# Kernel tuning notes

Measured on AMD Instinct MI355X. Metric: run time of the kernel, lower is better.

## Reference

```python
import math
import jax, jax.numpy as jnp
import numpy as np

ORIG_FREQ = 16000
NEW_FREQ = 14400
LPF_WIDTH = 6


def _kaldi_weights(orig_freq, new_freq, lpf_width):
    """Kaldi LinearResample SetIndexesAndWeights (numpy, static)."""
    base = math.gcd(orig_freq, new_freq)
    output_samples = new_freq // base
    min_freq = min(orig_freq, new_freq)
    lowpass_cutoff = 0.99 * 0.5 * min_freq
    window_width = lpf_width / (2.0 * lowpass_cutoff)
    output_t = np.arange(output_samples, dtype=np.float64) / new_freq
    min_t = output_t - window_width
    max_t = output_t + window_width
    min_input_index = np.ceil(min_t * orig_freq)
    max_input_index = np.floor(max_t * orig_freq)
    num_indices = max_input_index - min_input_index + 1
    max_weight_width = int(num_indices.max())
    j = np.arange(max_weight_width, dtype=np.float64)
    input_index = min_input_index[:, None] + j[None, :]
    delta_t = input_index / orig_freq - output_t[:, None]
    weights = np.zeros_like(delta_t)
    inside = np.abs(delta_t) < window_width
    weights[inside] = 0.5 * (1 + np.cos(2 * math.pi * lowpass_cutoff / lpf_width * delta_t[inside]))
    t_zero = delta_t == 0.0
    t_nz = ~t_zero
    weights[t_nz] *= np.sin(2 * math.pi * lowpass_cutoff * delta_t[t_nz]) / (math.pi * delta_t[t_nz])
    weights[t_zero] *= 2 * lowpass_cutoff
    weights /= orig_freq
    return min_input_index.astype(np.int64), weights.astype(np.float32)


def _output_samples(input_num_samp, orig_freq, new_freq):
    tick_freq = abs(orig_freq * new_freq) // math.gcd(orig_freq, new_freq)
    ticks_per_input = tick_freq // orig_freq
    interval_length = input_num_samp * ticks_per_input
    if interval_length <= 0:
        return 0
    ticks_per_output = tick_freq // new_freq
    last = interval_length // ticks_per_output
    if last * ticks_per_output == interval_length:
        last -= 1
    return last + 1


def setup_inputs() -> dict:
    key = jax.random.key(0)
    waveforms = jax.random.normal(key, (64, 480000), dtype=jnp.float32)
    return {"waveforms": waveforms}


def reference(waveforms) -> jnp.ndarray:
    B, T = waveforms.shape
    base = math.gcd(ORIG_FREQ, NEW_FREQ)
    conv_stride = ORIG_FREQ // base          # input samples per unit (10)
    up = NEW_FREQ // base                    # output phases (9)
    first_indices, weights_np = _kaldi_weights(ORIG_FREQ, NEW_FREQ, LPF_WIDTH)
    window_size = weights_np.shape[1]
    tot_out = _output_samples(T, ORIG_FREQ, NEW_FREQ)
    max_index = (tot_out - 1) // up
    end_index = max_index * conv_stride + window_size

    x3 = waveforms[:, None, :]  # [B, 1, T]
    out = jnp.zeros((B, tot_out), dtype=waveforms.dtype)
    dn = jax.lax.conv_dimension_numbers((B, 1, T), (1, 1, window_size), ('NCH', 'OIH', 'NCH'))
    for i in range(up):
        fi = int(first_indices[i])
        start = max(0, fi)
        left_pad = max(0, -fi)
        cur_len = T - fi
        right_pad = max(0, end_index + 1 - cur_len)
        xw = jnp.pad(x3[..., start:], ((0, 0), (0, 0), (left_pad, right_pad)))
        ker = jnp.asarray(weights_np[i], dtype=waveforms.dtype)[None, None, :]
        cw = jax.lax.conv_general_dilated(xw, ker, (conv_stride,), 'VALID', dimension_numbers=dn)[:, 0, :]
        # place phase-i outputs at positions i, i+up, i+2*up, ... < tot_out
        count = (tot_out - i + up - 1) // up
        cw = cw[:, :count]
        if cw.shape[1] < count:
            cw = jnp.pad(cw, ((0, 0), (0, count - cw.shape[1])))
        out = out.at[:, i::up].add(cw)
    return out
```

## Files before the change

### kernel.cpp

```cpp
#include <hip/hip_runtime.h>
#include <math.h>

#define T_IN        480000
#define OUT_PER_ROW 432000
#define K_TOT       48000
#define GPB         256
#define LDS_FLOATS  2576
#define OUT_LDS     (GPB * 9)

struct ResampleW { float w[9][14]; };

__global__ __launch_bounds__(256)
void SpeedPerturb_resample_kernel(const float* __restrict__ in,
                                  float* __restrict__ out,
                                  ResampleW args)
{
    __shared__ float lin[LDS_FLOATS];
    __shared__ float lout[OUT_LDS];
    const int row = blockIdx.y;
    const int k0  = blockIdx.x * GPB;
    const int t   = threadIdx.x;
    const int is0 = 10 * k0 - 6;
    const int al  = is0 & ~3;
    const int off = is0 - al;
    const float* rin = in + (size_t)row * T_IN;

    for (int q = t; q < LDS_FLOATS / 4; q += 256) {
        const int g0 = al + 4 * q;
        float4 v;
        if (g0 >= 0 && g0 + 3 < T_IN) {
            v = *reinterpret_cast<const float4*>(rin + g0);
        } else {
            v.x = (g0 + 0 >= 0 && g0 + 0 < T_IN) ? rin[g0 + 0] : 0.f;
            v.y = (g0 + 1 >= 0 && g0 + 1 < T_IN) ? rin[g0 + 1] : 0.f;
            v.z = (g0 + 2 >= 0 && g0 + 2 < T_IN) ? rin[g0 + 2] : 0.f;
            v.w = (g0 + 3 >= 0 && g0 + 3 < T_IN) ? rin[g0 + 3] : 0.f;
        }
        *reinterpret_cast<float4*>(&lin[4 * q]) = v;
    }
    __syncthreads();

    const int k = k0 + t;
    if (k < K_TOT) {
        float v[24];
        const int base = off + 10 * t;
        #pragma unroll
        for (int m = 0; m < 12; ++m) {
            float2 p = *reinterpret_cast<const float2*>(&lin[base + 2 * m]);
            v[2 * m]     = p.x;
            v[2 * m + 1] = p.y;
        }

        constexpr int RB[9] = {0, 1, 2, 3, 4, 5, 6, 8, 9};

        #pragma unroll
        for (int i = 0; i < 9; ++i) {
            float s = 0.f;
            #pragma unroll
            for (int j = 0; j < 14; ++j)
                s = fmaf(args.w[i][j], v[RB[i] + j], s);
            lout[9 * t + i] = s;
        }
    }
    __syncthreads();

    const int nout = min(OUT_LDS, (K_TOT - k0) * 9);
    float* obase = out + (size_t)row * OUT_PER_ROW + (size_t)k0 * 9;
    for (int q = t; q < nout / 4; q += 256) {
        *reinterpret_cast<float4*>(obase + 4 * q) =
            *reinterpret_cast<const float4*>(&lout[4 * q]);
    }
}

extern "C" void kernel_launch(void* const* d_in, const int* in_sizes, int n_in,
                              void* d_out, int out_size, void* d_ws, size_t ws_size,
                              hipStream_t stream) {
    const float* in  = (const float*)d_in[0];
    float*       out = (float*)d_out;
    const int B = out_size / OUT_PER_ROW;

    ResampleW args;
    const double orig = 16000.0;
    const double lowpass_cutoff = 0.99 * 0.5 * 14400.0;
    const double window_width = 6.0 / (2.0 * lowpass_cutoff);
    const double PI = 3.14159265358979323846;
    for (int i = 0; i < 9; ++i) {
        const double output_t = (double)i / 14400.0;
        const double min_input_index = ceil((output_t - window_width) * orig);
        for (int j = 0; j < 14; ++j) {
            const double delta_t = (min_input_index + j) / orig - output_t;
            double w = 0.0;
            if (fabs(delta_t) < window_width) {
                w = 0.5 * (1.0 + cos(2.0 * PI * lowpass_cutoff / 6.0 * delta_t));
                if (delta_t != 0.0)
                    w *= sin(2.0 * PI * lowpass_cutoff * delta_t) / (PI * delta_t);
                else
                    w *= 2.0 * lowpass_cutoff;
                w /= orig;
            }
            args.w[i][j] = (float)w;
        }
    }

    dim3 grid((K_TOT + GPB - 1) / GPB, B);
    SpeedPerturb_resample_kernel<<<grid, dim3(256), 0, stream>>>(in, out, args);
}
```

Before: 210.8 us.

## Load input directly into registers and compute two groups per thread

Removes the LDS staging buffer for the input waveform. Each thread now reads its 36-sample window straight from global memory with aligned float4 loads, and edge blocks fall back to scalar bounds-checked loads. Each thread handles two output groups, which halves the grid and drops one barrier. The cost is overlapping global reads between neighbouring threads, which rely on the cache, plus higher register pressure.

```diff
diff --git a/kernel.cpp b/kernel.cpp
--- a/kernel.cpp
+++ b/kernel.cpp
@@ -4,9 +4,9 @@
 #define T_IN        480000
 #define OUT_PER_ROW 432000
 #define K_TOT       48000
-#define GPB         256
-#define LDS_FLOATS  2576
-#define OUT_LDS     (GPB * 9)
+#define PAIRS_PB    256
+#define GROUPS_PB   (2 * PAIRS_PB)
+#define OUT_LDS     (GROUPS_PB * 9)
 
 struct ResampleW { float w[9][14]; };
 
@@ -15,58 +15,52 @@
                                   float* __restrict__ out,
                                   ResampleW args)
 {
-    __shared__ float lin[LDS_FLOATS];
     __shared__ float lout[OUT_LDS];
     const int row = blockIdx.y;
-    const int k0  = blockIdx.x * GPB;
+    const int k0  = blockIdx.x * GROUPS_PB;
     const int t   = threadIdx.x;
-    const int is0 = 10 * k0 - 6;
-    const int al  = is0 & ~3;
-    const int off = is0 - al;
+    const int kp  = (k0 >> 1) + t;
     const float* rin = in + (size_t)row * T_IN;
 
-    for (int q = t; q < LDS_FLOATS / 4; q += 256) {
-        const int g0 = al + 4 * q;
-        float4 v;
-        if (g0 >= 0 && g0 + 3 < T_IN) {
-            v = *reinterpret_cast<const float4*>(rin + g0);
-        } else {
-            v.x = (g0 + 0 >= 0 && g0 + 0 < T_IN) ? rin[g0 + 0] : 0.f;
-            v.y = (g0 + 1 >= 0 && g0 + 1 < T_IN) ? rin[g0 + 1] : 0.f;
-            v.z = (g0 + 2 >= 0 && g0 + 2 < T_IN) ? rin[g0 + 2] : 0.f;
-            v.w = (g0 + 3 >= 0 && g0 + 3 < T_IN) ? rin[g0 + 3] : 0.f;
+    const int al = 20 * kp - 8;
+    float v[36];
+    const bool interior = (blockIdx.x > 0) && (blockIdx.x < gridDim.x - 1);
+    if (interior) {
+        #pragma unroll
+        for (int m = 0; m < 9; ++m) {
+            float4 q = *reinterpret_cast<const float4*>(rin + al + 4 * m);
+            v[4 * m + 0] = q.x; v[4 * m + 1] = q.y;
+            v[4 * m + 2] = q.z; v[4 * m + 3] = q.w;
         }
-        *reinterpret_cast<float4*>(&lin[4 * q]) = v;
+    } else {
+        #pragma unroll
+        for (int m = 0; m < 36; ++m) {
+            const int idx = al + m;
+            v[m] = (idx >= 0 && idx < T_IN) ? rin[idx] : 0.f;
+        }
     }
-    __syncthreads();
 
-    const int k = k0 + t;
-    if (k < K_TOT) {
-        float v[24];
-        const int base = off + 10 * t;
-        #pragma unroll
-        for (int m = 0; m < 12; ++m) {
-            float2 p = *reinterpret_cast<const float2*>(&lin[base + 2 * m]);
-            v[2 * m]     = p.x;
-            v[2 * m + 1] = p.y;
-        }
+    constexpr int RB[9] = {0, 1, 2, 3, 4, 5, 6, 8, 9};
 
-        constexpr int RB[9] = {0, 1, 2, 3, 4, 5, 6, 8, 9};
-
-        #pragma unroll
-        for (int i = 0; i < 9; ++i) {
-            float s = 0.f;
+    #pragma unroll
+    for (int g = 0; g < 2; ++g) {
+        const int k = k0 + 2 * t + g;
+        if (k < K_TOT) {
             #pragma unroll
-            for (int j = 0; j < 14; ++j)
-                s = fmaf(args.w[i][j], v[RB[i] + j], s);
-            lout[9 * t + i] = s;
+            for (int i = 0; i < 9; ++i) {
+                float s = 0.f;
+                #pragma unroll
+                for (int j = 0; j < 14; ++j)
+                    s = fmaf(args.w[i][j], v[2 + 10 * g + RB[i] + j], s);
+                lout[18 * t + 9 * g + i] = s;
+            }
         }
     }
     __syncthreads();
 
     const int nout = min(OUT_LDS, (K_TOT - k0) * 9);
     float* obase = out + (size_t)row * OUT_PER_ROW + (size_t)k0 * 9;
-    for (int q = t; q < nout / 4; q += 256) {
+    for (int q = t; q < (nout >> 2); q += 256) {
         *reinterpret_cast<float4*>(obase + 4 * q) =
             *reinterpret_cast<const float4*>(&lout[4 * q]);
     }
@@ -102,6 +96,6 @@
         }
     }
 
-    dim3 grid((K_TOT + GPB - 1) / GPB, B);
+    dim3 grid((K_TOT + GROUPS_PB - 1) / GROUPS_PB, B);
     SpeedPerturb_resample_kernel<<<grid, dim3(256), 0, stream>>>(in, out, args);
 }
```

New measurement: 210.5 us. No clear change (-0.2%).
